# Performance work log

Hardware: AMD Instinct MI355X
Metric: run time of the kernel (lower is better)

## Reference

```python
import jax, jax.numpy as jnp
import numpy as np

B, S, DIM, EXTRA, NK, NH, NL = 16, 256, 41, 1, 128, 4, 3
ND = DIM + EXTRA  # 42 channels after appending the Time2Vec extra channel


def _lin(key, fin, fout):
    kw, kb = jax.random.split(key)
    w = jax.random.normal(kw, (fin, fout), jnp.float32) / np.float32(np.sqrt(fin))
    b = jax.random.normal(kb, (fout,), jnp.float32) * 0.01
    return w, b


def _stack(key, fin, fout):
    ws, bs = zip(*[_lin(k, fin, fout) for k in jax.random.split(key, NL)])
    return jnp.stack(ws), jnp.stack(bs)


def setup_inputs():
    key = jax.random.key(0)
    ks = jax.random.split(key, 32)
    inp = {}
    inp['context_x'] = jnp.sort(jax.random.uniform(ks[0], (B, S), jnp.float32), axis=1)
    inp['value'] = jax.random.normal(ks[1], (B, S, DIM), jnp.float32)
    mask = (jax.random.uniform(ks[2], (B, S, DIM)) < 0.23).astype(jnp.float32)
    inp['mask'] = mask
    inp['target_value'] = jax.random.normal(ks[3], (B, S, DIM), jnp.float32)
    inp['target_mask'] = mask * (jax.random.uniform(ks[4], (B, S, DIM)) < 0.3).astype(jnp.float32)
    inp['t2v_w0'] = jax.random.normal(ks[5], (1,), jnp.float32)
    inp['t2v_b0'] = jax.random.normal(ks[6], (1,), jnp.float32)
    inp['edge_w'], inp['edge_b'] = _lin(ks[7], 2, NK)
    inp['chan_w'], inp['chan_b'] = _lin(ks[8], ND, NK)
    inp['time_w'], inp['time_b'] = _lin(ks[9], 1, NK)
    base = 10
    for pre, dk in (('ct', 2 * NK), ('tc', 2 * NK), ('ca', NK)):
        inp[pre + '_wq'], inp[pre + '_bq'] = _stack(ks[base], NK, NK); base += 1
        inp[pre + '_wk'], inp[pre + '_bk'] = _stack(ks[base], dk, NK); base += 1
        inp[pre + '_wv'], inp[pre + '_bv'] = _stack(ks[base], dk, NK); base += 1
        inp[pre + '_wo'], inp[pre + '_bo'] = _stack(ks[base], NK, NK); base += 1
    inp['en_w'], inp['en_b'] = _stack(ks[base], 3 * NK, NK); base += 1
    inp['out_w'], inp['out_b'] = _lin(ks[base], 3 * NK, 1)
    return inp


def _mab2(Q, K, wq, bq, wk, bk, wv, bv, wo, bo, mask):
    # GraFITi MAB2: fc_q/fc_k/fc_v -> dim_out, multihead attn, O = Q + A@V, then O += relu(fc_o(O))
    q = Q @ wq + bq
    k = K @ wk + bk
    v = K @ wv + bv
    b, nq, d = q.shape
    dh = d // NH
    qh = q.reshape(b, nq, NH, dh)
    kh = k.reshape(b, -1, NH, dh)
    vh = v.reshape(b, -1, NH, dh)
    att = jnp.einsum('bqhd,bkhd->bhqk', qh, kh) / np.float32(np.sqrt(d))
    if mask is not None:
        att = jnp.where(mask[:, None] == 0, jnp.float32(-1e10), att)
    A = jax.nn.softmax(att, axis=-1)
    o = (qh + jnp.einsum('bhqk,bkhd->bqhd', A, vh)).reshape(b, nq, d)
    return o + jax.nn.relu(o @ wo + bo)


def _forward(context_x, value, mask, target_value, target_mask, t2v_w0, t2v_b0,
             edge_w, edge_b, chan_w, chan_b, time_w, time_b,
             ct_wq, ct_bq, ct_wk, ct_bk, ct_wv, ct_bv, ct_wo, ct_bo,
             tc_wq, tc_bq, tc_wk, tc_bk, tc_wv, tc_bv, tc_wo, tc_bo,
             en_w, en_b,
             ca_wq, ca_bq, ca_wk, ca_bk, ca_wv, ca_bv, ca_wo, ca_bo,
             out_w, out_b):
    te = (t2v_w0 * context_x + t2v_b0)[:, :, None]  # Time2Vec linear channel [B,S,1]
    value_f = jnp.concatenate([value, te], -1)  # [B,S,ND]
    mask_f = jnp.concatenate([mask, jnp.ones((B, S, EXTRA), jnp.float32)], -1)
    tval_f = jnp.concatenate([target_value, te], -1)
    tmask_f = jnp.concatenate([target_mask, jnp.zeros((B, S, EXTRA), jnp.float32)], -1)
    # ragged compaction: observed entries first, zero-padded to the batch max count
    full_len = int(np.asarray(jnp.max(jnp.sum(mask_f, axis=(1, 2)))))
    order = jnp.argsort(-mask_f.reshape(B, -1), axis=1, stable=True)[:, :full_len]
    take = lambda x: jnp.take_along_axis(x.reshape(B, -1), order, axis=1)
    mk_ = take(mask_f)  # [B,L]: ones then zero padding
    U_val = take(value_f) * mk_
    target_U_ = take(tval_f) * mk_
    target_mask_ = take(tmask_f) * mk_
    mki = mk_.astype(jnp.int32)
    T_inds_ = take(jnp.broadcast_to(jnp.arange(S, dtype=jnp.int32)[None, :, None], (B, S, ND))) * mki
    C_inds_ = take(jnp.broadcast_to(jnp.arange(ND, dtype=jnp.int32)[None, None, :], (B, S, ND))) * mki
    C_mask = (C_inds_[:, None, :] == jnp.arange(ND)[None, :, None]).astype(jnp.float32) * mk_[:, None, :]
    T_mask = (T_inds_[:, None, :] == jnp.arange(S)[None, :, None]).astype(jnp.float32) * mk_[:, None, :]
    U_ind = 1.0 - mk_ + target_mask_
    U = jax.nn.relu(jnp.stack([U_val, U_ind], -1) @ edge_w + edge_b) * mk_[:, :, None]  # [B,L,NK]
    T_ = jnp.sin(context_x[:, :, None] @ time_w + time_b)  # [B,S,NK]
    # one_hot(arange(ND)) @ chan_w == chan_w
    C_ = jnp.broadcast_to(jax.nn.relu(chan_w + chan_b)[None], (B, ND, NK))
    gT = lambda x, idx: jnp.take_along_axis(x, jnp.broadcast_to(idx[:, :, None], (B, full_len, NK)), axis=1)
    for i in range(NL):
        k_t = gT(T_, T_inds_)
        C2 = _mab2(C_, jnp.concatenate([k_t, U], -1), ct_wq[i], ct_bq[i], ct_wk[i], ct_bk[i], ct_wv[i], ct_bv[i], ct_wo[i], ct_bo[i], C_mask)
        k_c = gT(C_, C_inds_)
        T2 = _mab2(T_, jnp.concatenate([k_c, U], -1), tc_wq[i], tc_bq[i], tc_wk[i], tc_bk[i], tc_wv[i], tc_bv[i], tc_wo[i], tc_bo[i], T_mask)
        U = jax.nn.relu(U + jnp.concatenate([U, k_t, k_c], -1) @ en_w[i] + en_b[i]) * mk_[:, :, None]
        C_ = _mab2(C2, C2, ca_wq[i], ca_bq[i], ca_wk[i], ca_bk[i], ca_wv[i], ca_bv[i], ca_wo[i], ca_bo[i], None)
        T_ = T2
    k_t = gT(T_, T_inds_)
    k_c = gT(C_, C_inds_)
    output = jnp.concatenate([U, k_t, k_c], -1) @ out_w + out_b  # [B,L,1]
    return output, target_U_, target_mask_


def reference(context_x, value, mask, target_value, target_mask, t2v_w0, t2v_b0, edge_w, edge_b, chan_w, chan_b, time_w, time_b, ct_wq, ct_bq, ct_wk, ct_bk, ct_wv, ct_bv, ct_wo, ct_bo, tc_wq, tc_bq, tc_wk, tc_bk, tc_wv, tc_bv, tc_wo, tc_bo, en_w, en_b, ca_wq, ca_bq, ca_wk, ca_bk, ca_wv, ca_bv, ca_wo, ca_bo, out_w, out_b):
    return _forward(context_x, value, mask, target_value, target_mask, t2v_w0, t2v_b0, edge_w, edge_b, chan_w, chan_b, time_w, time_b, ct_wq, ct_bq, ct_wk, ct_bk, ct_wv, ct_bv, ct_wo, ct_bo, tc_wq, tc_bq, tc_wk, tc_bk, tc_wv, tc_bv, tc_wo, tc_bo, en_w, en_b, ca_wq, ca_bq, ca_wk, ca_bk, ca_wv, ca_bv, ca_wo, ca_bo, out_w, out_b)
```

## Files before the change

### kernel.cpp

```cpp
#include <hip/hip_runtime.h>
#include <math.h>

#define NB   16
#define SS   256
#define DIMV 41
#define NDV  42
#define NKD  128
#define NHD  4
#define DH   32
#define NLAY 3
#define TOT  (SS*NDV)
#define NCH  42

typedef __attribute__((ext_vector_type(8))) short short8;
typedef __attribute__((ext_vector_type(4))) float floatx4;

__device__ __forceinline__ short f2bf(float x) {
    unsigned u = __float_as_uint(x);
    u += 0x7fff + ((u >> 16) & 1);
    return (short)(u >> 16);
}
__device__ __forceinline__ float bf2f(unsigned s) {
    return __uint_as_float(s << 16);
}

struct Seg { const float* ptr; const int* ind; int ns; };

__device__ __forceinline__ const float* seg_row(const Seg s, int gm, int Lb) {
    if (s.ind) {
        int b = gm / Lb;
        int id = s.ind[gm]; if (id < 0) id = 0;
        return s.ptr + ((size_t)b * s.ns + (size_t)id) * NKD;
    }
    return s.ptr + (size_t)gm * NKD;
}


__device__ __forceinline__ void compactA_body(int bx, const float* __restrict__ maskp,
                                              int* __restrict__ chunkcnt)
{
    const int b = bx / NCH, ch = bx % NCH;
    const int tid = threadIdx.x;
    const int idx = ch * 256 + tid;
    const int s = idx / NDV, c = idx % NDV;
    float m = (c < DIMV) ? maskp[((size_t)b*SS + s)*DIMV + c] : 1.0f;
    int x = (m != 0.0f) ? 1 : 0;
    #pragma unroll
    for (int off = 32; off; off >>= 1) x += __shfl_down(x, off);
    __shared__ int ws4[4];
    if ((tid & 63) == 0) ws4[tid >> 6] = x;
    __syncthreads();
    if (tid == 0) chunkcnt[bx] = ws4[0] + ws4[1] + ws4[2] + ws4[3];
}

__device__ __forceinline__ void zero_body(int bx, int* __restrict__ lo_t,
                                          int* __restrict__ hi_t)
{
    int i = bx*256 + threadIdx.x;
    if (i < NB*SS) { lo_t[i] = 0; hi_t[i] = 0; }
}

__device__ __forceinline__ void initT_body(int bx, const float* __restrict__ cx,
                                           const float* __restrict__ tw,
                                           const float* __restrict__ tb,
                                           float* __restrict__ T)
{
    int i = bx * 256 + threadIdx.x;
    if (i >= NB*SS*32) return;
    int row = i >> 5;
    int k = (i & 31) << 2;
    float t = cx[row];
    float4 r;
    r.x = sinf(t*tw[k+0] + tb[k+0]);
    r.y = sinf(t*tw[k+1] + tb[k+1]);
    r.z = sinf(t*tw[k+2] + tb[k+2]);
    r.w = sinf(t*tw[k+3] + tb[k+3]);
    *(float4*)(T + (size_t)row*NKD + k) = r;
}

__device__ __forceinline__ void initC_body(int bx, const float* __restrict__ cw,
                                           const float* __restrict__ cb,
                                           float* __restrict__ C)
{
    int i = bx * 256 + threadIdx.x;
    if (i >= NB*NDV*32) return;
    int row = i >> 5;
    int c = row % NDV;
    int k = (i & 31) << 2;
    float4 r;
    r.x = fmaxf(cw[(size_t)c*NKD + k+0] + cb[k+0], 0.f);
    r.y = fmaxf(cw[(size_t)c*NKD + k+1] + cb[k+1], 0.f);
    r.z = fmaxf(cw[(size_t)c*NKD + k+2] + cb[k+2], 0.f);
    r.w = fmaxf(cw[(size_t)c*NKD + k+3] + cb[k+3], 0.f);
    *(float4*)(C + (size_t)row*NKD + k) = r;
}

template<int Kg>
__device__ __forceinline__ void prep1(const float* __restrict__ src,
                                      short* __restrict__ dst, int rel)
{
    const int per = Kg*128;
    int i = rel / per; int r2 = rel - i*per;
    int n = r2 / Kg;   int k = r2 - n*Kg;
    dst[rel] = f2bf(src[(size_t)i*per + (size_t)k*128 + n]);
}

#define W_TOTAL 933888
__device__ __forceinline__ void prepw_body(int bx,
    const float* ctq, const float* ctk, const float* ctv, const float* cto,
    const float* tcq, const float* tck, const float* tcv, const float* tco,
    const float* caq, const float* cak, const float* cav, const float* cao,
    const float* enw, short* __restrict__ arena)
{
    int idx = bx*256 + threadIdx.x;
    if (idx >= W_TOTAL) return;
    if      (idx < 49152 ) prep1<128>(ctq, arena + 0,      idx - 0);
    else if (idx < 147456) prep1<256>(ctk, arena + 49152,  idx - 49152);
// ... 48 lines not shown
            base[c] = run; clo[b*NDV + c] = run;
            run += hist[c]; chi[b*NDV + c] = run;
        }
        cntsh = run;
    }
    __syncthreads();
    if (tid < NDV) hist[tid] = 0;
    __syncthreads();
    const int cnt = cntsh;
    for (int l = tid; l < L; l += 256) {
        int c = cind[(size_t)b*L + l];
        int pos;
        if (c >= 0) pos = base[c] + atomicAdd(&hist[c], 1);
        else        pos = cnt + atomicAdd(&padc, 1);
        invp[(size_t)b*L + l] = b*L + pos;
    }
}

__device__ __forceinline__ void initU_body(int bx, const float* __restrict__ uval,
                                           const float* __restrict__ uind,
                                           const float* __restrict__ mkb,
                                           const float* __restrict__ ew,
                                           const float* __restrict__ eb,
                                           float* __restrict__ U, int BL)
{
    int i = bx * 256 + threadIdx.x;
    if (i >= BL*32) return;
    int row = i >> 5;
    int k = (i & 31) << 2;
    float uv = uval[row], ui = uind[row], m = mkb[row];
    float4 r;
    r.x = fmaxf(uv*ew[k+0] + ui*ew[NKD+k+0] + eb[k+0], 0.f) * m;
    r.y = fmaxf(uv*ew[k+1] + ui*ew[NKD+k+1] + eb[k+1], 0.f) * m;
    r.z = fmaxf(uv*ew[k+2] + ui*ew[NKD+k+2] + eb[k+2], 0.f) * m;
    r.w = fmaxf(uv*ew[k+3] + ui*ew[NKD+k+3] + eb[k+3], 0.f) * m;
    *(float4*)(U + (size_t)row*NKD + k) = r;
}

template<int NSEG, int MODE>
__device__ __forceinline__ void mgemm_body(char* smem, int bx,
           Seg s0, Seg s1, Seg s2, const short* __restrict__ Wt,
           const float* __restrict__ bias, float* __restrict__ D,
           int M, int Lb, const float* __restrict__ mkp)
{
    short (*As)[40] = (short (*)[40])smem;
    short (*Bs)[40] = (short (*)[40])(smem + 10240);
    const int bm = bx * 128;
    const int tid = threadIdx.x;
    const int wv = tid >> 6;
    const int lane = tid & 63;
    const int quad = lane >> 4;
    const int l16 = lane & 15;
    const int K = NSEG * 128;
    floatx4 acc[2][8];
    #pragma unroll
    for (int i = 0; i < 2; i++)
        #pragma unroll
        for (int j = 0; j < 8; j++) acc[i][j] = (floatx4){0.f,0.f,0.f,0.f};

    const int arow = tid >> 1;
    const int acol = (tid & 1) * 16;
    int gmc = bm + arow; if (gmc > M-1) gmc = M-1;
    const float* rowp0 = seg_row(s0, gmc, Lb);
    const float* rowp1 = (NSEG > 1) ? seg_row(s1, gmc, Lb) : nullptr;
    const float* rowp2 = (NSEG > 2) ? seg_row(s2, gmc, Lb) : nullptr;

    for (int k0 = 0; k0 < K; k0 += 32) {
        {
            const float* rp;
            if (NSEG == 1) rp = rowp0;
            else if (NSEG == 2) rp = (k0 < 128) ? rowp0 : rowp1;
            else rp = (k0 < 128) ? rowp0 : ((k0 < 256) ? rowp1 : rowp2);
            const int ks = k0 & 127;
            const float* src = rp + ks + acol;
            float4 a0 = *(const float4*)(src);
            float4 a1 = *(const float4*)(src+4);
            float4 a2 = *(const float4*)(src+8);
            float4 a3 = *(const float4*)(src+12);
            short8 p0, p1;
            p0[0]=f2bf(a0.x); p0[1]=f2bf(a0.y); p0[2]=f2bf(a0.z); p0[3]=f2bf(a0.w);
            p0[4]=f2bf(a1.x); p0[5]=f2bf(a1.y); p0[6]=f2bf(a1.z); p0[7]=f2bf(a1.w);
            p1[0]=f2bf(a2.x); p1[1]=f2bf(a2.y); p1[2]=f2bf(a2.z); p1[3]=f2bf(a2.w);
            p1[4]=f2bf(a3.x); p1[5]=f2bf(a3.y); p1[6]=f2bf(a3.z); p1[7]=f2bf(a3.w);
            *(short8*)&As[arow][acol]   = p0;
            *(short8*)&As[arow][acol+8] = p1;
        }
        {
            const short* src = Wt + (size_t)arow*K + k0 + acol;
            *(short8*)&Bs[arow][acol]   = *(const short8*)(src);
            *(short8*)&Bs[arow][acol+8] = *(const short8*)(src+8);
        }
        __syncthreads();
        short8 af0 = *(short8*)&As[wv*32 + l16][quad*8];
        short8 af1 = *(short8*)&As[wv*32 + 16 + l16][quad*8];
        #pragma unroll
        for (int nf = 0; nf < 8; nf++) {
            short8 bf = *(short8*)&Bs[nf*16 + l16][quad*8];
            acc[0][nf] = __builtin_amdgcn_mfma_f32_16x16x32_bf16(af0, bf, acc[0][nf], 0, 0, 0);
            acc[1][nf] = __builtin_amdgcn_mfma_f32_16x16x32_bf16(af1, bf, acc[1][nf], 0, 0, 0);
        }
        __syncthreads();
    }
    #pragma unroll
    for (int mf = 0; mf < 2; mf++) {
        #pragma unroll
        for (int r = 0; r < 4; r++) {
            int gm = bm + wv*32 + mf*16 + quad*4 + r;
            if (gm < M) {
                float mk = (MODE == 3) ? mkp[gm] : 0.f;
                const float* res = (MODE == 2 || MODE == 3) ? seg_row(s0, gm, Lb) : nullptr;
                #pragma unroll
                for (int nf = 0; nf < 8; nf++) {
                    int gn = nf*16 + l16;
                    float val = acc[mf][nf][r] + bias[gn];
                    if (MODE == 2) val = res[gn] + fmaxf(val, 0.f);
                    else if (MODE == 3) val = fmaxf(res[gn] + val, 0.f) * mk;
                    D[(size_t)gm*NKD + gn] = val;
                }
            }
        }
    }
}

template<int NSEG, bool HASQ>
__device__ __forceinline__ void mgemm_kv_body(char* smem, int bx,
              Seg s0, Seg s1,
              const short* __restrict__ Wk, const float* __restrict__ bk,
              const short* __restrict__ Wv, const float* __restrict__ bv,
              const short* __restrict__ Wq, const float* __restrict__ bq,
              float* __restrict__ Qd,
              unsigned* __restrict__ KV, int M, int Lb, const int* __restrict__ rmap)
{
    short (*As)[40] = (short (*)[40])smem;
    short (*Bk_)[40] = (short (*)[40])(smem + 5120);
    short (*Bv_)[40] = (short (*)[40])(smem + 15360);
    short (*Bq_)[40] = (short (*)[40])(smem + 25600);
    const int bm = bx * 64;
    const int tid = threadIdx.x;
    const int wv = tid >> 6;
    const int lane = tid & 63;
    const int quad = lane >> 4;
    const int l16 = lane & 15;
    const int K = NSEG * 128;
    floatx4 acck[8], accv[8], accq[8];
    #pragma unroll
    for (int j = 0; j < 8; j++) {
        acck[j] = (floatx4){0.f,0.f,0.f,0.f};
        accv[j] = (floatx4){0.f,0.f,0.f,0.f};
        if (HASQ) accq[j] = (floatx4){0.f,0.f,0.f,0.f};
    }

    const int arow = tid >> 2;
    const int acol = (tid & 3) * 8;
    const int brow = tid >> 1;
    const int bcol = (tid & 1) * 16;
    int gmc = bm + arow; if (gmc > M-1) gmc = M-1;
    const float* rowp0 = seg_row(s0, gmc, Lb);
    const float* rowp1 = (NSEG > 1) ? seg_row(s1, gmc, Lb) : nullptr;

    for (int k0 = 0; k0 < K; k0 += 32) {
        {
            const float* rp = (NSEG == 1) ? rowp0 : ((k0 < 128) ? rowp0 : rowp1);
            const int ks = k0 & 127;
            const float* src = rp + ks + acol;
            float4 a0 = *(const float4*)(src);
            float4 a1 = *(const float4*)(src+4);
            short8 p0;
            p0[0]=f2bf(a0.x); p0[1]=f2bf(a0.y); p0[2]=f2bf(a0.z); p0[3]=f2bf(a0.w);
            p0[4]=f2bf(a1.x); p0[5]=f2bf(a1.y); p0[6]=f2bf(a1.z); p0[7]=f2bf(a1.w);
            *(short8*)&As[arow][acol] = p0;
        }
        {
            const short* sk = Wk + (size_t)brow*K + k0 + bcol;
            *(short8*)&Bk_[brow][bcol]   = *(const short8*)(sk);
            *(short8*)&Bk_[brow][bcol+8] = *(const short8*)(sk+8);
            const short* sv = Wv + (size_t)brow*K + k0 + bcol;
            *(short8*)&Bv_[brow][bcol]   = *(const short8*)(sv);
            *(short8*)&Bv_[brow][bcol+8] = *(const short8*)(sv+8);
            if (HASQ) {
                const short* sq = Wq + (size_t)brow*K + k0 + bcol;
                *(short8*)&Bq_[brow][bcol]   = *(const short8*)(sq);
                *(short8*)&Bq_[brow][bcol+8] = *(const short8*)(sq+8);
            }
        }
        __syncthreads();
        short8 af = *(short8*)&As[wv*16 + l16][quad*8];
        #pragma unroll
        for (int nf = 0; nf < 8; nf++) {
            short8 bfk = *(short8*)&Bk_[nf*16 + l16][quad*8];
            acck[nf] = __builtin_amdgcn_mfma_f32_16x16x32_bf16(af, bfk, acck[nf], 0, 0, 0);
            short8 bfv = *(short8*)&Bv_[nf*16 + l16][quad*8];
            accv[nf] = __builtin_amdgcn_mfma_f32_16x16x32_bf16(af, bfv, accv[nf], 0, 0, 0);
            if (HASQ) {
                short8 bfq = *(short8*)&Bq_[nf*16 + l16][quad*8];
                accq[nf] = __builtin_amdgcn_mfma_f32_16x16x32_bf16(af, bfq, accq[nf], 0, 0, 0);
            }
        }
        __syncthreads();
    }
    #pragma unroll
    for (int r = 0; r < 4; r++) {
        int gm = bm + wv*16 + quad*4 + r;
        if (gm < M) {
            int orow = rmap ? rmap[gm] : gm;
            #pragma unroll
            for (int nf = 0; nf < 8; nf++) {
                int gn = nf*16 + l16;
                float kf = acck[nf][r] + bk[gn];
                float vf = accv[nf][r] + bv[gn];
                unsigned pk = (unsigned)(unsigned short)f2bf(kf)
                            | ((unsigned)(unsigned short)f2bf(vf) << 16);
                KV[(size_t)orow*NKD + gn] = pk;
                if (HASQ) Qd[(size_t)gm*NKD + gn] = accq[nf][r] + bq[gn];
            }
        }
    }
}

template<int SPLIT>
__device__ __forceinline__ void sattn_body(int bx,
                  const float* __restrict__ q, const unsigned* __restrict__ kvb,
                  float* __restrict__ o, int nq, int nkv,
                  const int* __restrict__ lo_arr, const int* __restrict__ hi_arr)
{
    __shared__ float sm_m[4], sm_s[4], sm_a[4][DH];
    const int wvid = threadIdx.x >> 6;
    int gtask = bx * 4 + wvid;
    int task = gtask / SPLIT;
    int part = gtask % SPLIT;
    if (task >= NB * nq * NHD) return;
    const int h = task & 3;
    const int bq = task >> 2;
    const int qi = bq % nq;
    const int b = bq / nq;
    const int lane = threadIdx.x & 63;
    const int d = lane & 31;
    const int half = lane >> 5;
    int lo = lo_arr ? lo_arr[b*nq + qi] : 0;
    int hi = hi_arr ? hi_arr[b*nq + qi] : nkv;
    if (SPLIT == 2) {
        int mid = lo + ((hi - lo + 1) >> 1);
        if (part == 0) hi = mid; else lo = mid;
    }
    const float scale = 0.088388347648318447f;

    const float qv = q[((size_t)(b*nq + qi))*NKD + h*DH + d];
    const unsigned* kb = kvb + (size_t)b*nkv*NKD + h*DH + d;

    float m = -INFINITY, ssum = 0.f, acc = 0.f;
    for (int l0 = lo; l0 < hi; l0 += 8) {
        unsigned ur[4];
        #pragma unroll
        for (int j = 0; j < 4; j++) {
            int l = l0 + 2*j + half;
            bool ok = (l < hi);
            ur[j] = ok ? kb[(size_t)l*NKD] : 0u;
        }
        #pragma unroll
        for (int j = 0; j < 4; j++) {
            int l = l0 + 2*j + half;
            float kr = bf2f(ur[j] & 0xffffu);
            float vr = bf2f(ur[j] >> 16);
            float partial = qv * kr;
            #pragma unroll
            for (int off = 16; off; off >>= 1) partial += __shfl_xor(partial, off);
            float s = partial * scale;
            if (l < hi) {
                float mn = fmaxf(m, s);
                float corr = __expf(m - mn);
                float p = __expf(s - mn);
                ssum = ssum * corr + p;
                acc  = acc  * corr + p * vr;
                m = mn;
            }
        }
    }
    float mo = __shfl_xor(m, 32);
    float M = fmaxf(m, mo);
    float corr = (m > -1e30f) ? __expf(m - M) : 0.f;
    ssum *= corr; acc *= corr;
    ssum += __shfl_xor(ssum, 32);
    acc  += __shfl_xor(acc, 32);

    if (SPLIT == 1) {
        if (half == 0) {
            float res = (ssum > 0.f) ? acc / ssum : 0.f;
            o[((size_t)(b*nq + qi))*NKD + h*DH + d] = qv + res;
        }
    } else {
        if (lane == 0) { sm_m[wvid] = M; sm_s[wvid] = ssum; }
        if (lane < DH) sm_a[wvid][lane] = acc;
        __syncthreads();
        if (part == 0 && lane < DH) {
            float m2 = sm_m[wvid+1], s2 = sm_s[wvid+1], a2 = sm_a[wvid+1][lane];
            float M2 = fmaxf(M, m2);
            float c1 = (M  > -1e30f) ? __expf(M  - M2) : 0.f;
            float c2 = (m2 > -1e30f) ? __expf(m2 - M2) : 0.f;
            float S = ssum * c1 + s2 * c2;
            float A = acc  * c1 + a2 * c2;
            float res = (S > 0.f) ? A / S : 0.f;
            o[((size_t)(b*nq + qi))*NKD + h*DH + lane] = qv + res;
        }
    }
}


__global__ __launch_bounds__(256)
void k_pre1(const float* maskp, int* chunkcnt, int* lo_t, int* hi_t,
            const float* cx, const float* tw, const float* tb, float* T,
            const float* cw, const float* cb, float* C,
            const float* ctq, const float* ctk, const float* ctv, const float* cto,
            const float* tcq, const float* tck, const float* tcv, const float* tco,
            const float* caq, const float* cak, const float* cav, const float* cao,
            const float* enw, short* arena)
{
    int bx = blockIdx.x;
    if (bx < NB*NCH)            compactA_body(bx, maskp, chunkcnt);
    else if (bx < NB*NCH + 16)  zero_body(bx - NB*NCH, lo_t, hi_t);
    else if (bx < NB*NCH + 16 + 512) initT_body(bx - NB*NCH - 16, cx, tw, tb, T);
    else if (bx < NB*NCH + 16 + 512 + 84) initC_body(bx - NB*NCH - 16 - 512, cw, cb, C);
    else prepw_body(bx - NB*NCH - 16 - 512 - 84,
                    ctq, ctk, ctv, cto, tcq, tck, tcv, tco,
                    caq, cak, cav, cao, enw, arena);
}

__global__ __launch_bounds__(64)
void k_compactB(const int* __restrict__ chunkcnt, int* __restrict__ chunkoff,
                int* __restrict__ cntb)
{
    const int b = blockIdx.x, lane = threadIdx.x;
    int v = (lane < NCH) ? chunkcnt[b*NCH + lane] : 0;
    int x = v;
    #pragma unroll
    for (int off = 1; off < 64; off <<= 1) {
        int y = __shfl_up(x, off);
        if (lane >= off) x += y;
    }
    if (lane < NCH) chunkoff[b*NCH + lane] = x - v;
    if (lane == 63) cntb[b] = x;
}

__global__ __launch_bounds__(256)
void k_compactC(const float* __restrict__ cx, const float* __restrict__ value,
              const float* __restrict__ maskp, const float* __restrict__ tval,
// ... 32 lines not shown
        float te = w0 * cx[(size_t)b*SS + s] + b0;
        float vf, tvf, tmf;
        if (c < DIMV) {
            size_t o = ((size_t)b*SS + s)*DIMV + c;
            vf = value[o]; tvf = tval[o]; tmf = tmaskp[o];
        } else { vf = te; tvf = te; tmf = 0.0f; }
        size_t p = (size_t)b*L + pos;
        if (m) {
            tind[p] = s; cind[p] = c; mkb[p] = 1.0f;
            uval[p] = vf; uind[p] = tmf;
            outTU[p] = tvf; outTM[p] = tmf;
        } else {
            tind[p] = -1; cind[p] = -1; mkb[p] = 0.0f;
            uval[p] = 0.0f; uind[p] = 1.0f;
            outTU[p] = 0.0f; outTM[p] = 0.0f;
        }
    }
}

__global__ __launch_bounds__(256)
void k_pre4(const int* tind, int* lo_t, int* hi_t, int L, int gTr,
            const int* cind, int* invp, int* clo, int* chi,
            const float* uval, const float* uind, const float* mkb,
            const float* ew, const float* eb, float* U, int BL)
{
    int bx = blockIdx.x;
    if (bx < gTr) trange_body(bx, tind, lo_t, hi_t, L);
    else if (bx < gTr + NB) cperm_body(bx - gTr, cind, invp, clo, chi, L);
    else initU_body(bx - gTr - NB, uval, uind, mkb, ew, eb, U, BL);
}

__global__ __launch_bounds__(256)
void k_phase1(int g0, int g1, int g2, int g3,
              const float* T1, const int* tind, const float* U,
              const short* wkct, const float* bkct, const short* wvct, const float* bvct,
              unsigned* KVct, const int* invp,
              const float* C1, const short* wqct, const float* bqct, float* qC,
              const int* cind,
              const short* wktc, const float* bktc, const short* wvtc, const float* bvtc,
              unsigned* KVtc,
              const short* wqtc, const float* bqtc, float* qT,
              const short* wen, const float* ben, float* Unew, const float* mkb,
              int BL, int L)
{
    __shared__ __align__(16) char smem[25600];
    int bx = blockIdx.x;
    if (bx < g0) {
        mgemm_kv_body<2,false>(smem, bx, Seg{T1,tind,SS}, Seg{U,nullptr,0},
            wkct, bkct, wvct, bvct, nullptr, nullptr, nullptr, KVct, BL, L, invp);
    } else if (bx < g0+g1) {
        mgemm_body<1,0>(smem, bx-g0, Seg{C1,nullptr,0}, Seg{nullptr,nullptr,0},
            Seg{nullptr,nullptr,0}, wqct, bqct, qC, NB*NDV, 1, nullptr);
    } else if (bx < g0+g1+g2) {
        mgemm_kv_body<2,false>(smem, bx-g0-g1, Seg{C1,cind,NDV}, Seg{U,nullptr,0},
            wktc, bktc, wvtc, bvtc, nullptr, nullptr, nullptr, KVtc, BL, L, nullptr);
    } else if (bx < g0+g1+g2+g3) {
        mgemm_body<1,0>(smem, bx-g0-g1-g2, Seg{T1,nullptr,0}, Seg{nullptr,nullptr,0},
            Seg{nullptr,nullptr,0}, wqtc, bqtc, qT, NB*SS, 1, nullptr);
    } else {
        mgemm_body<3,3>(smem, bx-g0-g1-g2-g3, Seg{U,nullptr,0}, Seg{T1,tind,SS},
            Seg{C1,cind,NDV}, wen, ben, Unew, BL, L, mkb);
    }
}

__global__ __launch_bounds__(256)
void k_phase2(int g0, const float* qC, const unsigned* KVct, float* oC,
              const int* clo, const int* chi, int L,
              const float* qT, const unsigned* KVtc, float* oT,
              const int* lo_t, const int* hi_t)
{
    int bx = blockIdx.x;
    if (bx < g0) sattn_body<2>(bx, qC, KVct, oC, NDV, L, clo, chi);
    else         sattn_body<1>(bx-g0, qT, KVtc, oT, SS, L, lo_t, hi_t);
}

__global__ __launch_bounds__(256)
void k_phase3(int g0, const float* oC, const short* woct, const float* boct, float* C2,
              const float* oT, const short* wotc, const float* botc, float* T2b)
{
    __shared__ __align__(16) char smem[20480];
    int bx = blockIdx.x;
    if (bx < g0)
        mgemm_body<1,2>(smem, bx, Seg{oC,nullptr,0}, Seg{nullptr,nullptr,0},
            Seg{nullptr,nullptr,0}, woct, boct, C2, NB*NDV, 1, nullptr);
    else
        mgemm_body<1,2>(smem, bx-g0, Seg{oT,nullptr,0}, Seg{nullptr,nullptr,0},
            Seg{nullptr,nullptr,0}, wotc, botc, T2b, NB*SS, 1, nullptr);
}

__global__ __launch_bounds__(256)
void k_ca_kvq(const float* C2, const short* wk, const float* bk,
              const short* wv, const float* bv, const short* wq, const float* bq,
              float* qC, unsigned* KV)
{
    __shared__ __align__(16) char smem[35840];
    mgemm_kv_body<1,true>(smem, blockIdx.x, Seg{C2,nullptr,0}, Seg{nullptr,nullptr,0},
                          wk, bk, wv, bv, wq, bq, qC, KV, NB*NDV, 1, nullptr);
}

__global__ __launch_bounds__(256)
void k_ca_attn(const float* qC, const unsigned* kv, float* oC)
{
    sattn_body<2>(blockIdx.x, qC, kv, oC, NDV, NDV, nullptr, nullptr);
}

__global__ __launch_bounds__(256)
void k_ca_oproj(const float* oC, const short* wo, const float* bo, float* C1)
{
    __shared__ __align__(16) char smem[20480];
    mgemm_body<1,2>(smem, blockIdx.x, Seg{oC,nullptr,0}, Seg{nullptr,nullptr,0},
                    Seg{nullptr,nullptr,0}, wo, bo, C1, NB*NDV, 1, nullptr);
}

__global__ __launch_bounds__(256)
void k_out(const float* __restrict__ U, const float* __restrict__ T1,
           const float* __restrict__ C1, const int* __restrict__ tind,
           const int* __restrict__ cind, const float* __restrict__ ow,
           const float* __restrict__ obp, float* __restrict__ out,
           int BL, int L)
{
    int row = blockIdx.x * 4 + (threadIdx.x >> 6);
    int lane = threadIdx.x & 63;
    if (row >= BL) return;
    int b = row / L;
    int ti = tind[row]; if (ti < 0) ti = 0;
    int ci = cind[row]; if (ci < 0) ci = 0;
    const float* u = U + (size_t)row*NKD;
    const float* a = T1 + ((size_t)(b*SS + ti))*NKD;
    const float* c = C1 + ((size_t)(b*NDV + ci))*NKD;
    float s = u[lane]*ow[lane]       + u[lane+64]*ow[lane+64]
            + a[lane]*ow[128+lane]   + a[lane+64]*ow[192+lane]
            + c[lane]*ow[256+lane]   + c[lane+64]*ow[320+lane];
    #pragma unroll
    for (int off = 32; off; off >>= 1) s += __shfl_down(s, off);
    if (lane == 0) out[row] = s + obp[0];
}

extern "C" void kernel_launch(void* const* d_in, const int* in_sizes, int n_in,
                              void* d_out, int out_size, void* d_ws, size_t ws_size,
                              hipStream_t stream)
{
    const float* cx     = (const float*)d_in[0];
    const float* value  = (const float*)d_in[1];
    const float* maskp  = (const float*)d_in[2];
    const float* tval   = (const float*)d_in[3];
    const float* tmaskp = (const float*)d_in[4];
    const float* w0     = (const float*)d_in[5];
    const float* b0     = (const float*)d_in[6];
    const float* edge_w = (const float*)d_in[7];
    const float* edge_b = (const float*)d_in[8];
    const float* chan_w = (const float*)d_in[9];
    const float* chan_b = (const float*)d_in[10];
    const float* time_w = (const float*)d_in[11];
    const float* time_b = (const float*)d_in[12];
    const float* ct_wq = (const float*)d_in[13];
// ... 24 lines not shown
    const float* en_b  = (const float*)d_in[38];
    const float* out_w = (const float*)d_in[39];
    const float* out_b = (const float*)d_in[40];

    const int BL = out_size / 3;
    const int L  = BL / NB;

    char* p = (char*)d_ws;
    auto alloc = [&](size_t n) { char* r = p; p += (n + 255) & ~(size_t)255; return r; };
    int*      tind   = (int*)  alloc((size_t)BL*4);
    int*      cind   = (int*)  alloc((size_t)BL*4);
    float*    mkb    = (float*)alloc((size_t)BL*4);
    float*    uval   = (float*)alloc((size_t)BL*4);
    float*    uind   = (float*)alloc((size_t)BL*4);
    int*      lo_t   = (int*)  alloc((size_t)NB*SS*4);
    int*      hi_t   = (int*)  alloc((size_t)NB*SS*4);
    int*      clo    = (int*)  alloc((size_t)NB*NDV*4);
    int*      chi    = (int*)  alloc((size_t)NB*NDV*4);
    int*      invp   = (int*)  alloc((size_t)BL*4);
    int*      chunkc = (int*)  alloc((size_t)NB*NCH*4);
    int*      chunko = (int*)  alloc((size_t)NB*NCH*4);
    int*      cntb   = (int*)  alloc((size_t)NB*4);
    short*    waren  = (short*)alloc((size_t)W_TOTAL*2);
    float*    U    = (float*)alloc((size_t)BL*NKD*4);
    float*    Unew = (float*)alloc((size_t)BL*NKD*4);
    unsigned* KVct = (unsigned*)alloc((size_t)BL*NKD*4);
    unsigned* KVtc = (unsigned*)alloc((size_t)BL*NKD*4);
    unsigned* kvCa = (unsigned*)alloc((size_t)NB*NDV*NKD*4);
    float*    T1   = (float*)alloc((size_t)NB*SS*NKD*4);
    float*    T2b  = (float*)alloc((size_t)NB*SS*NKD*4);
    float*    qT   = (float*)alloc((size_t)NB*SS*NKD*4);
    float*    oT   = (float*)alloc((size_t)NB*SS*NKD*4);
    float*    C1   = (float*)alloc((size_t)NB*NDV*NKD*4);
    float*    C2   = (float*)alloc((size_t)NB*NDV*NKD*4);
    float*    qC   = (float*)alloc((size_t)NB*NDV*NKD*4);
    float*    oC   = (float*)alloc((size_t)NB*NDV*NKD*4);

    float* outMain = (float*)d_out;
    float* outTU = outMain + BL;
    float* outTM = outMain + 2*BL;

    const size_t OCTQ=0, OCTK=49152, OCTV=147456, OCTO=245760;
    const size_t OTCQ=294912, OTCK=344064, OTCV=442368, OTCO=540672;
    const size_t OCAQ=589824, OCAK=638976, OCAV=688128, OCAO=737280, OEN=786432;

    k_pre1<<<NB*NCH + 16 + 512 + 84 + W_TOTAL/256, 256, 0, stream>>>(
        maskp, chunkc, lo_t, hi_t, cx, time_w, time_b, T1, chan_w, chan_b, C1,
        ct_wq, ct_wk, ct_wv, ct_wo, tc_wq, tc_wk, tc_wv, tc_wo,
        ca_wq, ca_wk, ca_wv, ca_wo, en_w, waren);
    k_compactB<<<NB, 64, 0, stream>>>(chunkc, chunko, cntb);
    k_compactC<<<NB*NCH, 256, 0, stream>>>(cx, value, maskp, tval, tmaskp, w0, b0,
                                           chunko, cntb, L, tind, cind, mkb, uval, uind,
                                           outTU, outTM);
    {
        const int gTr = (NB*L + 255)/256;
        const int gU  = (BL*32 + 255)/256;
        k_pre4<<<gTr + NB + gU, 256, 0, stream>>>(
            tind, lo_t, hi_t, L, gTr, cind, invp, clo, chi,
            uval, uind, mkb, edge_w, edge_b, U, BL);
    }

    const int gBL  = (BL + 127)/128;
    const int gKV  = (BL + 63)/64;
    const int gC   = (NB*NDV + 127)/128;
    const int gT   = (NB*SS + 127)/128;
    const int gCa  = (NB*NDV + 63)/64;
    const int aC2  = NB*NDV*NHD*2/4;
    const int aTC  = NB*SS*NHD/4;

    for (int i = 0; i < NLAY; i++) {
        const size_t bOff = (size_t)i*NKD;
        const short* wq_ct = waren + OCTQ + (size_t)i*128*128;
        const short* wk_ct = waren + OCTK + (size_t)i*256*128;
        const short* wv_ct = waren + OCTV + (size_t)i*256*128;
        const short* wo_ct = waren + OCTO + (size_t)i*128*128;
        const short* wq_tc = waren + OTCQ + (size_t)i*128*128;
        const short* wk_tc = waren + OTCK + (size_t)i*256*128;
        const short* wv_tc = waren + OTCV + (size_t)i*256*128;
        const short* wo_tc = waren + OTCO + (size_t)i*128*128;
        const short* wq_ca = waren + OCAQ + (size_t)i*128*128;
        const short* wk_ca = waren + OCAK + (size_t)i*128*128;
        const short* wv_ca = waren + OCAV + (size_t)i*128*128;
        const short* wo_ca = waren + OCAO + (size_t)i*128*128;
        const short* w_en  = waren + OEN  + (size_t)i*384*128;

        k_phase1<<<gKV + gC + gKV + gT + gBL, 256, 0, stream>>>(
            gKV, gC, gKV, gT,
            T1, tind, U,
            wk_ct, ct_bk + bOff, wv_ct, ct_bv + bOff, KVct, invp,
            C1, wq_ct, ct_bq + bOff, qC,
            cind, wk_tc, tc_bk + bOff, wv_tc, tc_bv + bOff, KVtc,
            wq_tc, tc_bq + bOff, qT,
            w_en, en_b + bOff, Unew, mkb, BL, L);
        k_phase2<<<aC2 + aTC, 256, 0, stream>>>(
            aC2, qC, KVct, oC, clo, chi, L, qT, KVtc, oT, lo_t, hi_t);
        k_phase3<<<gC + gT, 256, 0, stream>>>(
            gC, oC, wo_ct, ct_bo + bOff, C2, oT, wo_tc, tc_bo + bOff, T2b);
        k_ca_kvq<<<gCa, 256, 0, stream>>>(C2, wk_ca, ca_bk + bOff,
            wv_ca, ca_bv + bOff, wq_ca, ca_bq + bOff, qC, kvCa);
        k_ca_attn<<<aC2, 256, 0, stream>>>(qC, kvCa, oC);
        k_ca_oproj<<<gC, 256, 0, stream>>>(oC, wo_ca, ca_bo + bOff, C1);

        float* t = U;  U = Unew; Unew = t;
        t = T1; T1 = T2b; T2b = t;
    }

    k_out<<<(BL + 3)/4, 256, 0, stream>>>(U, T1, C1, tind, cind,
                                          out_w, out_b, outMain, BL, L);
}
```

Baseline: 490.1 us.

## Store intermediate activations as bf16 and move U-update GEMM into phase3

All intermediate activation buffers (T, C, U, q, attention outputs) switch from fp32 to bf16 storage. GEMM A-tile loads become direct short8 copies with no per-element conversion, and epilogues round to bf16 on write. This halves activation memory traffic and removes conversion work, but adds extra rounding of residual paths across layers. The encoder U-update GEMM also moves from phase1 to phase3, a different launch, to rebalance block counts across the fused launches.

```diff
diff --git a/kernel.cpp b/kernel.cpp
--- a/kernel.cpp
+++ b/kernel.cpp
@@ -20,13 +20,16 @@
     u += 0x7fff + ((u >> 16) & 1);
     return (short)(u >> 16);
 }
+__device__ __forceinline__ float bfs2f(short s) {
+    return __uint_as_float(((unsigned)(unsigned short)s) << 16);
+}
 __device__ __forceinline__ float bf2f(unsigned s) {
     return __uint_as_float(s << 16);
 }
 
-struct Seg { const float* ptr; const int* ind; int ns; };
-
-__device__ __forceinline__ const float* seg_row(const Seg s, int gm, int Lb) {
+struct Seg { const short* ptr; const int* ind; int ns; };
+
+__device__ __forceinline__ const short* seg_row(const Seg s, int gm, int Lb) {
     if (s.ind) {
         int b = gm / Lb;
         int id = s.ind[gm]; if (id < 0) id = 0;
@@ -63,36 +66,32 @@
 __device__ __forceinline__ void initT_body(int bx, const float* __restrict__ cx,
                                            const float* __restrict__ tw,
                                            const float* __restrict__ tb,
-                                           float* __restrict__ T)
+                                           short* __restrict__ T)
 {
     int i = bx * 256 + threadIdx.x;
-    if (i >= NB*SS*32) return;
-    int row = i >> 5;
-    int k = (i & 31) << 2;
+    if (i >= NB*SS*16) return;
+    int row = i >> 4;
+    int k = (i & 15) << 3;
     float t = cx[row];
-    float4 r;
-    r.x = sinf(t*tw[k+0] + tb[k+0]);
-    r.y = sinf(t*tw[k+1] + tb[k+1]);
-    r.z = sinf(t*tw[k+2] + tb[k+2]);
-    r.w = sinf(t*tw[k+3] + tb[k+3]);
-    *(float4*)(T + (size_t)row*NKD + k) = r;
+    short8 r;
+    #pragma unroll
+    for (int j = 0; j < 8; j++) r[j] = f2bf(sinf(t*tw[k+j] + tb[k+j]));
+    *(short8*)(T + (size_t)row*NKD + k) = r;
 }
 
 __device__ __forceinline__ void initC_body(int bx, const float* __restrict__ cw,
                                            const float* __restrict__ cb,
-                                           float* __restrict__ C)
+                                           short* __restrict__ C)
 {
     int i = bx * 256 + threadIdx.x;
-    if (i >= NB*NDV*32) return;
-    int row = i >> 5;
+    if (i >= NB*NDV*16) return;
+    int row = i >> 4;
     int c = row % NDV;
-    int k = (i & 31) << 2;
-    float4 r;
-    r.x = fmaxf(cw[(size_t)c*NKD + k+0] + cb[k+0], 0.f);
-    r.y = fmaxf(cw[(size_t)c*NKD + k+1] + cb[k+1], 0.f);
-    r.z = fmaxf(cw[(size_t)c*NKD + k+2] + cb[k+2], 0.f);
-    r.w = fmaxf(cw[(size_t)c*NKD + k+3] + cb[k+3], 0.f);
-    *(float4*)(C + (size_t)row*NKD + k) = r;
+    int k = (i & 15) << 3;
+    short8 r;
+    #pragma unroll
+    for (int j = 0; j < 8; j++) r[j] = f2bf(fmaxf(cw[(size_t)c*NKD + k+j] + cb[k+j], 0.f));
+    *(short8*)(C + (size_t)row*NKD + k) = r;
 }
 
 template<int Kg>
@@ -187,25 +186,24 @@
                                            const float* __restrict__ mkb,
                                            const float* __restrict__ ew,
                                            const float* __restrict__ eb,
-                                           float* __restrict__ U, int BL)
+                                           short* __restrict__ U, int BL)
 {
     int i = bx * 256 + threadIdx.x;
-    if (i >= BL*32) return;
-    int row = i >> 5;
-    int k = (i & 31) << 2;
+    if (i >= BL*16) return;
+    int row = i >> 4;
+    int k = (i & 15) << 3;
     float uv = uval[row], ui = uind[row], m = mkb[row];
-    float4 r;
-    r.x = fmaxf(uv*ew[k+0] + ui*ew[NKD+k+0] + eb[k+0], 0.f) * m;
-    r.y = fmaxf(uv*ew[k+1] + ui*ew[NKD+k+1] + eb[k+1], 0.f) * m;
-    r.z = fmaxf(uv*ew[k+2] + ui*ew[NKD+k+2] + eb[k+2], 0.f) * m;
-    r.w = fmaxf(uv*ew[k+3] + ui*ew[NKD+k+3] + eb[k+3], 0.f) * m;
-    *(float4*)(U + (size_t)row*NKD + k) = r;
+    short8 r;
+    #pragma unroll
+    for (int j = 0; j < 8; j++)
+        r[j] = f2bf(fmaxf(uv*ew[k+j] + ui*ew[NKD+k+j] + eb[k+j], 0.f) * m);
+    *(short8*)(U + (size_t)row*NKD + k) = r;
 }
 
 template<int NSEG, int MODE>
 __device__ __forceinline__ void mgemm_body(char* smem, int bx,
            Seg s0, Seg s1, Seg s2, const short* __restrict__ Wt,
-           const float* __restrict__ bias, float* __restrict__ D,
+           const float* __restrict__ bias, short* __restrict__ D,
            int M, int Lb, const float* __restrict__ mkp)
 {
     short (*As)[40] = (short (*)[40])smem;
@@ -226,29 +224,20 @@
     const int arow = tid >> 1;
     const int acol = (tid & 1) * 16;
     int gmc = bm + arow; if (gmc > M-1) gmc = M-1;
-    const float* rowp0 = seg_row(s0, gmc, Lb);
-    const float* rowp1 = (NSEG > 1) ? seg_row(s1, gmc, Lb) : nullptr;
-    const float* rowp2 = (NSEG > 2) ? seg_row(s2, gmc, Lb) : nullptr;
+    const short* rowp0 = seg_row(s0, gmc, Lb);
+    const short* rowp1 = (NSEG > 1) ? seg_row(s1, gmc, Lb) : nullptr;
+    const short* rowp2 = (NSEG > 2) ? seg_row(s2, gmc, Lb) : nullptr;
 
     for (int k0 = 0; k0 < K; k0 += 32) {
         {
-            const float* rp;
+            const short* rp;
             if (NSEG == 1) rp = rowp0;
             else if (NSEG == 2) rp = (k0 < 128) ? rowp0 : rowp1;
             else rp = (k0 < 128) ? rowp0 : ((k0 < 256) ? rowp1 : rowp2);
             const int ks = k0 & 127;
-            const float* src = rp + ks + acol;
-            float4 a0 = *(const float4*)(src);
-            float4 a1 = *(const float4*)(src+4);
-            float4 a2 = *(const float4*)(src+8);
-            float4 a3 = *(const float4*)(src+12);
-            short8 p0, p1;
-            p0[0]=f2bf(a0.x); p0[1]=f2bf(a0.y); p0[2]=f2bf(a0.z); p0[3]=f2bf(a0.w);
-            p0[4]=f2bf(a1.x); p0[5]=f2bf(a1.y); p0[6]=f2bf(a1.z); p0[7]=f2bf(a1.w);
-            p1[0]=f2bf(a2.x); p1[1]=f2bf(a2.y); p1[2]=f2bf(a2.z); p1[3]=f2bf(a2.w);
-            p1[4]=f2bf(a3.x); p1[5]=f2bf(a3.y); p1[6]=f2bf(a3.z); p1[7]=f2bf(a3.w);
-            *(short8*)&As[arow][acol]   = p0;
-            *(short8*)&As[arow][acol+8] = p1;
+            const short* src = rp + ks + acol;
+            *(short8*)&As[arow][acol]   = *(const short8*)(src);
+            *(short8*)&As[arow][acol+8] = *(const short8*)(src+8);
         }
         {
             const short* src = Wt + (size_t)arow*K + k0 + acol;
@@ -273,14 +262,14 @@
             int gm = bm + wv*32 + mf*16 + quad*4 + r;
             if (gm < M) {
                 float mk = (MODE == 3) ? mkp[gm] : 0.f;
-                const float* res = (MODE == 2 || MODE == 3) ? seg_row(s0, gm, Lb) : nullptr;
+                const short* res = (MODE == 2 || MODE == 3) ? seg_row(s0, gm, Lb) : nullptr;
                 #pragma unroll
                 for (int nf = 0; nf < 8; nf++) {
                     int gn = nf*16 + l16;
                     float val = acc[mf][nf][r] + bias[gn];
-                    if (MODE == 2) val = res[gn] + fmaxf(val, 0.f);
-                    else if (MODE == 3) val = fmaxf(res[gn] + val, 0.f) * mk;
-                    D[(size_t)gm*NKD + gn] = val;
+                    if (MODE == 2) val = bfs2f(res[gn]) + fmaxf(val, 0.f);
+                    else if (MODE == 3) val = fmaxf(bfs2f(res[gn]) + val, 0.f) * mk;
+                    D[(size_t)gm*NKD + gn] = f2bf(val);
                 }
             }
         }
@@ -293,7 +282,7 @@
               const short* __restrict__ Wk, const float* __restrict__ bk,
               const short* __restrict__ Wv, const float* __restrict__ bv,
               const short* __restrict__ Wq, const float* __restrict__ bq,
-              float* __restrict__ Qd,
+              short* __restrict__ Qd,
               unsigned* __restrict__ KV, int M, int Lb, const int* __restrict__ rmap)
 {
     short (*As)[40] = (short (*)[40])smem;
@@ -320,20 +309,14 @@
     const int brow = tid >> 1;
     const int bcol = (tid & 1) * 16;
     int gmc = bm + arow; if (gmc > M-1) gmc = M-1;
-    const float* rowp0 = seg_row(s0, gmc, Lb);
-    const float* rowp1 = (NSEG > 1) ? seg_row(s1, gmc, Lb) : nullptr;
+    const short* rowp0 = seg_row(s0, gmc, Lb);
+    const short* rowp1 = (NSEG > 1) ? seg_row(s1, gmc, Lb) : nullptr;
 
     for (int k0 = 0; k0 < K; k0 += 32) {
         {
-            const float* rp = (NSEG == 1) ? rowp0 : ((k0 < 128) ? rowp0 : rowp1);
+            const short* rp = (NSEG == 1) ? rowp0 : ((k0 < 128) ? rowp0 : rowp1);
             const int ks = k0 & 127;
-            const float* src = rp + ks + acol;
-            float4 a0 = *(const float4*)(src);
-            float4 a1 = *(const float4*)(src+4);
-            short8 p0;
-            p0[0]=f2bf(a0.x); p0[1]=f2bf(a0.y); p0[2]=f2bf(a0.z); p0[3]=f2bf(a0.w);
-            p0[4]=f2bf(a1.x); p0[5]=f2bf(a1.y); p0[6]=f2bf(a1.z); p0[7]=f2bf(a1.w);
-            *(short8*)&As[arow][acol] = p0;
+            *(short8*)&As[arow][acol] = *(const short8*)(rp + ks + acol);
         }
         {
             const short* sk = Wk + (size_t)brow*K + k0 + bcol;
@@ -376,7 +359,7 @@
                 unsigned pk = (unsigned)(unsigned short)f2bf(kf)
                             | ((unsigned)(unsigned short)f2bf(vf) << 16);
                 KV[(size_t)orow*NKD + gn] = pk;
-                if (HASQ) Qd[(size_t)gm*NKD + gn] = accq[nf][r] + bq[gn];
+                if (HASQ) Qd[(size_t)gm*NKD + gn] = f2bf(accq[nf][r] + bq[gn]);
             }
         }
     }
@@ -384,8 +367,8 @@
 
 template<int SPLIT>
 __device__ __forceinline__ void sattn_body(int bx,
-                  const float* __restrict__ q, const unsigned* __restrict__ kvb,
-                  float* __restrict__ o, int nq, int nkv,
+                  const short* __restrict__ q, const unsigned* __restrict__ kvb,
+                  short* __restrict__ o, int nq, int nkv,
                   const int* __restrict__ lo_arr, const int* __restrict__ hi_arr)
 {
     __shared__ float sm_m[4], sm_s[4], sm_a[4][DH];
@@ -409,7 +392,7 @@
     }
     const float scale = 0.088388347648318447f;
 
-    const float qv = q[((size_t)(b*nq + qi))*NKD + h*DH + d];
+    const float qv = bfs2f(q[((size_t)(b*nq + qi))*NKD + h*DH + d]);
     const unsigned* kb = kvb + (size_t)b*nkv*NKD + h*DH + d;
 
     float m = -INFINITY, ssum = 0.f, acc = 0.f;
@@ -450,7 +433,7 @@
     if (SPLIT == 1) {
         if (half == 0) {
             float res = (ssum > 0.f) ? acc / ssum : 0.f;
-            o[((size_t)(b*nq + qi))*NKD + h*DH + d] = qv + res;
+            o[((size_t)(b*nq + qi))*NKD + h*DH + d] = f2bf(qv + res);
         }
     } else {
         if (lane == 0) { sm_m[wvid] = M; sm_s[wvid] = ssum; }
@@ -464,7 +447,8 @@
             float S = ssum * c1 + s2 * c2;
             float A = acc  * c1 + a2 * c2;
             float res = (S > 0.f) ? A / S : 0.f;
-            o[((size_t)(b*nq + qi))*NKD + h*DH + lane] = qv + res;
+            float qv2 = bfs2f(q[((size_t)(b*nq + qi))*NKD + h*DH + lane]);
+            o[((size_t)(b*nq + qi))*NKD + h*DH + lane] = f2bf(qv2 + res);
         }
     }
 }
@@ -472,8 +456,8 @@
 
 __global__ __launch_bounds__(256)
 void k_pre1(const float* maskp, int* chunkcnt, int* lo_t, int* hi_t,
-            const float* cx, const float* tw, const float* tb, float* T,
-            const float* cw, const float* cb, float* C,
+            const float* cx, const float* tw, const float* tb, short* T,
+            const float* cw, const float* cb, short* C,
             const float* ctq, const float* ctk, const float* ctv, const float* cto,
             const float* tcq, const float* tck, const float* tcv, const float* tco,
             const float* caq, const float* cak, const float* cav, const float* cao,
@@ -482,9 +466,9 @@
     int bx = blockIdx.x;
     if (bx < NB*NCH)            compactA_body(bx, maskp, chunkcnt);
     else if (bx < NB*NCH + 16)  zero_body(bx - NB*NCH, lo_t, hi_t);
-    else if (bx < NB*NCH + 16 + 512) initT_body(bx - NB*NCH - 16, cx, tw, tb, T);
-    else if (bx < NB*NCH + 16 + 512 + 84) initC_body(bx - NB*NCH - 16 - 512, cw, cb, C);
-    else prepw_body(bx - NB*NCH - 16 - 512 - 84,
+    else if (bx < NB*NCH + 16 + 256) initT_body(bx - NB*NCH - 16, cx, tw, tb, T);
+    else if (bx < NB*NCH + 16 + 256 + 42) initC_body(bx - NB*NCH - 16 - 256, cw, cb, C);
+    else prepw_body(bx - NB*NCH - 16 - 256 - 42,
                     ctq, ctk, ctv, cto, tcq, tck, tcv, tco,
                     caq, cak, cav, cao, enw, arena);
 }
@@ -563,7 +547,7 @@
 void k_pre4(const int* tind, int* lo_t, int* hi_t, int L, int gTr,
             const int* cind, int* invp, int* clo, int* chi,
             const float* uval, const float* uind, const float* mkb,
-            const float* ew, const float* eb, float* U, int BL)
+            const float* ew, const float* eb, short* U, int BL)
 {
     int bx = blockIdx.x;
     if (bx < gTr) trange_body(bx, tind, lo_t, hi_t, L);
@@ -572,16 +556,15 @@
 }
 
 __global__ __launch_bounds__(256)
-void k_phase1(int g0, int g1, int g2, int g3,
-              const float* T1, const int* tind, const float* U,
+void k_phase1(int g0, int g1, int g2,
+              const short* T1, const int* tind, const short* U,
               const short* wkct, const float* bkct, const short* wvct, const float* bvct,
               unsigned* KVct, const int* invp,
-              const float* C1, const short* wqct, const float* bqct, float* qC,
+              const short* C1, const short* wqct, const float* bqct, short* qC,
               const int* cind,
               const short* wktc, const float* bktc, const short* wvtc, const float* bvtc,
               unsigned* KVtc,
-              const short* wqtc, const float* bqtc, float* qT,
-              const short* wen, const float* ben, float* Unew, const float* mkb,
+              const short* wqtc, const float* bqtc, short* qT,
               int BL, int L)
 {
     __shared__ __align__(16) char smem[25600];
@@ -595,19 +578,16 @@
     } else if (bx < g0+g1+g2) {
         mgemm_kv_body<2,false>(smem, bx-g0-g1, Seg{C1,cind,NDV}, Seg{U,nullptr,0},
             wktc, bktc, wvtc, bvtc, nullptr, nullptr, nullptr, KVtc, BL, L, nullptr);
-    } else if (bx < g0+g1+g2+g3) {
+    } else {
         mgemm_body<1,0>(smem, bx-g0-g1-g2, Seg{T1,nullptr,0}, Seg{nullptr,nullptr,0},
             Seg{nullptr,nullptr,0}, wqtc, bqtc, qT, NB*SS, 1, nullptr);
-    } else {
-        mgemm_body<3,3>(smem, bx-g0-g1-g2-g3, Seg{U,nullptr,0}, Seg{T1,tind,SS},
-            Seg{C1,cind,NDV}, wen, ben, Unew, BL, L, mkb);
-    }
-}
-
-__global__ __launch_bounds__(256)
-void k_phase2(int g0, const float* qC, const unsigned* KVct, float* oC,
+    }
+}
+
+__global__ __launch_bounds__(256)
+void k_phase2(int g0, const short* qC, const unsigned* KVct, short* oC,
               const int* clo, const int* chi, int L,
-              const float* qT, const unsigned* KVtc, float* oT,
+              const short* qT, const unsigned* KVtc, short* oT,
               const int* lo_t, const int* hi_t)
 {
     int bx = blockIdx.x;
@@ -616,23 +596,31 @@
 }
 
 __global__ __launch_bounds__(256)
-void k_phase3(int g0, const float* oC, const short* woct, const float* boct, float* C2,
-              const float* oT, const short* wotc, const float* botc, float* T2b)
+void k_phase3(int g0, int g1,
+              const short* oC, const short* woct, const float* boct, short* C2,
+              const short* oT, const short* wotc, const float* botc, short* T2b,
+              const short* U, const short* T1, const int* tind,
+              const short* C1, const int* cind,
+              const short* wen, const float* ben, short* Unew, const float* mkb,
+              int BL, int L)
 {
     __shared__ __align__(16) char smem[20480];
     int bx = blockIdx.x;
     if (bx < g0)
         mgemm_body<1,2>(smem, bx, Seg{oC,nullptr,0}, Seg{nullptr,nullptr,0},
             Seg{nullptr,nullptr,0}, woct, boct, C2, NB*NDV, 1, nullptr);
-    else
+    else if (bx < g0+g1)
         mgemm_body<1,2>(smem, bx-g0, Seg{oT,nullptr,0}, Seg{nullptr,nullptr,0},
             Seg{nullptr,nullptr,0}, wotc, botc, T2b, NB*SS, 1, nullptr);
-}
-
-__global__ __launch_bounds__(256)
-void k_ca_kvq(const float* C2, const short* wk, const float* bk,
+    else
+        mgemm_body<3,3>(smem, bx-g0-g1, Seg{U,nullptr,0}, Seg{T1,tind,SS},
+            Seg{C1,cind,NDV}, wen, ben, Unew, BL, L, mkb);
+}
+
+__global__ __launch_bounds__(256)
+void k_ca_kvq(const short* C2, const short* wk, const float* bk,
               const short* wv, const float* bv, const short* wq, const float* bq,
-              float* qC, unsigned* KV)
+              short* qC, unsigned* KV)
 {
     __shared__ __align__(16) char smem[35840];
     mgemm_kv_body<1,true>(smem, blockIdx.x, Seg{C2,nullptr,0}, Seg{nullptr,nullptr,0},
@@ -640,13 +628,13 @@
 }
 
 __global__ __launch_bounds__(256)
-void k_ca_attn(const float* qC, const unsigned* kv, float* oC)
+void k_ca_attn(const short* qC, const unsigned* kv, short* oC)
 {
     sattn_body<2>(blockIdx.x, qC, kv, oC, NDV, NDV, nullptr, nullptr);
 }
 
 __global__ __launch_bounds__(256)
-void k_ca_oproj(const float* oC, const short* wo, const float* bo, float* C1)
+void k_ca_oproj(const short* oC, const short* wo, const float* bo, short* C1)
 {
     __shared__ __align__(16) char smem[20480];
     mgemm_body<1,2>(smem, blockIdx.x, Seg{oC,nullptr,0}, Seg{nullptr,nullptr,0},
@@ -654,8 +642,8 @@
 }
 
 __global__ __launch_bounds__(256)
-void k_out(const float* __restrict__ U, const float* __restrict__ T1,
-           const float* __restrict__ C1, const int* __restrict__ tind,
+void k_out(const short* __restrict__ U, const short* __restrict__ T1,
+           const short* __restrict__ C1, const int* __restrict__ tind,
            const int* __restrict__ cind, const float* __restrict__ ow,
            const float* __restrict__ obp, float* __restrict__ out,
            int BL, int L)
@@ -666,12 +654,12 @@
     int b = row / L;
     int ti = tind[row]; if (ti < 0) ti = 0;
     int ci = cind[row]; if (ci < 0) ci = 0;
-    const float* u = U + (size_t)row*NKD;
-    const float* a = T1 + ((size_t)(b*SS + ti))*NKD;
-    const float* c = C1 + ((size_t)(b*NDV + ci))*NKD;
-    float s = u[lane]*ow[lane]       + u[lane+64]*ow[lane+64]
-            + a[lane]*ow[128+lane]   + a[lane+64]*ow[192+lane]
-            + c[lane]*ow[256+lane]   + c[lane+64]*ow[320+lane];
+    const short* u = U + (size_t)row*NKD;
+    const short* a = T1 + ((size_t)(b*SS + ti))*NKD;
+    const short* c = C1 + ((size_t)(b*NDV + ci))*NKD;
+    float s = bfs2f(u[lane])*ow[lane]     + bfs2f(u[lane+64])*ow[lane+64]
+            + bfs2f(a[lane])*ow[128+lane] + bfs2f(a[lane+64])*ow[192+lane]
+            + bfs2f(c[lane])*ow[256+lane] + bfs2f(c[lane+64])*ow[320+lane];
     #pragma unroll
     for (int off = 32; off; off >>= 1) s += __shfl_down(s, off);
     if (lane == 0) out[row] = s + obp[0];
@@ -742,19 +730,19 @@
     int*      chunko = (int*)  alloc((size_t)NB*NCH*4);
     int*      cntb   = (int*)  alloc((size_t)NB*4);
     short*    waren  = (short*)alloc((size_t)W_TOTAL*2);
-    float*    U    = (float*)alloc((size_t)BL*NKD*4);
-    float*    Unew = (float*)alloc((size_t)BL*NKD*4);
+    short*    U    = (short*)alloc((size_t)BL*NKD*2);
+    short*    Unew = (short*)alloc((size_t)BL*NKD*2);
     unsigned* KVct = (unsigned*)alloc((size_t)BL*NKD*4);
     unsigned* KVtc = (unsigned*)alloc((size_t)BL*NKD*4);
     unsigned* kvCa = (unsigned*)alloc((size_t)NB*NDV*NKD*4);
-    float*    T1   = (float*)alloc((size_t)NB*SS*NKD*4);
-    float*    T2b  = (float*)alloc((size_t)NB*SS*NKD*4);
-    float*    qT   = (float*)alloc((size_t)NB*SS*NKD*4);
-    float*    oT   = (float*)alloc((size_t)NB*SS*NKD*4);
-    float*    C1   = (float*)alloc((size_t)NB*NDV*NKD*4);
-    float*    C2   = (float*)alloc((size_t)NB*NDV*NKD*4);
-    float*    qC   = (float*)alloc((size_t)NB*NDV*NKD*4);
-    float*    oC   = (float*)alloc((size_t)NB*NDV*NKD*4);
+    short*    T1   = (short*)alloc((size_t)NB*SS*NKD*2);
+    short*    T2b  = (short*)alloc((size_t)NB*SS*NKD*2);
+    short*    qT   = (short*)alloc((size_t)NB*SS*NKD*2);
+    short*    oT   = (short*)alloc((size_t)NB*SS*NKD*2);
+    short*    C1   = (short*)alloc((size_t)NB*NDV*NKD*2);
+    short*    C2   = (short*)alloc((size_t)NB*NDV*NKD*2);
+    short*    qC   = (short*)alloc((size_t)NB*NDV*NKD*2);
+    short*    oC   = (short*)alloc((size_t)NB*NDV*NKD*2);
 
     float* outMain = (float*)d_out;
     float* outTU = outMain + BL;
@@ -764,7 +752,7 @@
     const size_t OTCQ=294912, OTCK=344064, OTCV=442368, OTCO=540672;
     const size_t OCAQ=589824, OCAK=638976, OCAV=688128, OCAO=737280, OEN=786432;
 
-    k_pre1<<<NB*NCH + 16 + 512 + 84 + W_TOTAL/256, 256, 0, stream>>>(
+    k_pre1<<<NB*NCH + 16 + 256 + 42 + W_TOTAL/256, 256, 0, stream>>>(
         maskp, chunkc, lo_t, hi_t, cx, time_w, time_b, T1, chan_w, chan_b, C1,
         ct_wq, ct_wk, ct_wv, ct_wo, tc_wq, tc_wk, tc_wv, tc_wo,
         ca_wq, ca_wk, ca_wv, ca_wo, en_w, waren);
@@ -774,7 +762,7 @@
                                            outTU, outTM);
     {
         const int gTr = (NB*L + 255)/256;
-        const int gU  = (BL*32 + 255)/256;
+        const int gU  = (BL*16 + 255)/256;
         k_pre4<<<gTr + NB + gU, 256, 0, stream>>>(
             tind, lo_t, hi_t, L, gTr, cind, invp, clo, chi,
             uval, uind, mkb, edge_w, edge_b, U, BL);
@@ -804,24 +792,24 @@
         const short* wo_ca = waren + OCAO + (size_t)i*128*128;
         const short* w_en  = waren + OEN  + (size_t)i*384*128;
 
-        k_phase1<<<gKV + gC + gKV + gT + gBL, 256, 0, stream>>>(
-            gKV, gC, gKV, gT,
+        k_phase1<<<gKV + gC + gKV + gT, 256, 0, stream>>>(
+            gKV, gC, gKV,
             T1, tind, U,
             wk_ct, ct_bk + bOff, wv_ct, ct_bv + bOff, KVct, invp,
             C1, wq_ct, ct_bq + bOff, qC,
             cind, wk_tc, tc_bk + bOff, wv_tc, tc_bv + bOff, KVtc,
-            wq_tc, tc_bq + bOff, qT,
-            w_en, en_b + bOff, Unew, mkb, BL, L);
+            wq_tc, tc_bq + bOff, qT, BL, L);
         k_phase2<<<aC2 + aTC, 256, 0, stream>>>(
             aC2, qC, KVct, oC, clo, chi, L, qT, KVtc, oT, lo_t, hi_t);
-        k_phase3<<<gC + gT, 256, 0, stream>>>(
-            gC, oC, wo_ct, ct_bo + bOff, C2, oT, wo_tc, tc_bo + bOff, T2b);
+        k_phase3<<<gC + gT + gBL, 256, 0, stream>>>(
+            gC, gT, oC, wo_ct, ct_bo + bOff, C2, oT, wo_tc, tc_bo + bOff, T2b,
+            U, T1, tind, C1, cind, w_en, en_b + bOff, Unew, mkb, BL, L);
         k_ca_kvq<<<gCa, 256, 0, stream>>>(C2, wk_ca, ca_bk + bOff,
             wv_ca, ca_bv + bOff, wq_ca, ca_bq + bOff, qC, kvCa);
         k_ca_attn<<<aC2, 256, 0, stream>>>(qC, kvCa, oC);
         k_ca_oproj<<<gC, 256, 0, stream>>>(oC, wo_ca, ca_bo + bOff, C1);
 
-        float* t = U;  U = Unew; Unew = t;
+        short* t = U;  U = Unew; Unew = t;
         t = T1; T1 = T2b; T2b = t;
     }
 
```

Result: faster. 468.2 us (-4.5%).
